# Optimization experiments

Measured on AMD Instinct MI355X. Metric: run time of the kernel, lower is better.

Reference implementation:

```python
import jax, jax.numpy as jnp
import numpy as np

B, S, D = 8, 2048, 1024
G, V = 2, 320          # num_groups, codebook_size
DG = D // G            # 512, per-group codevector dim
DIVERSITY_WEIGHT = 0.1


def setup_inputs() -> dict:
    key = jax.random.key(0)
    k1, k2, k3, k4 = jax.random.split(key, 4)
    hidden_states = jax.random.normal(k1, (B, S, D), dtype=jnp.float32)
    W = jax.random.normal(k2, (G * V, D), dtype=jnp.float32)   # weight_proj weight (torch Linear layout)
    b = jax.random.normal(k3, (G * V,), dtype=jnp.float32)     # weight_proj bias
    codevectors = jax.random.normal(k4, (1, G * V, DG), dtype=jnp.float32)
    return {"hidden_states": hidden_states, "W": W, "b": b, "codevectors": codevectors}


def reference(hidden_states, W, b, codevectors):
    batch, seq, _ = hidden_states.shape
    n_tok = batch * seq
    # weight_proj: [B,S,D] -> [B,S,G*V]
    logits = jnp.einsum("bsd,vd->bsv", hidden_states, W) + b
    logits_flat = logits.reshape(n_tok * G, V)
    # eval path: hard argmax codevector selection
    codevector_idx = jnp.argmax(logits_flat, axis=-1)          # [n_tok*G]
    probs = jax.nn.one_hot(codevector_idx, V, dtype=logits.dtype)  # exact one-hot, [n_tok*G, V]
    probs_g = probs.reshape(n_tok, G, V)
    # perplexity over marginal code usage (mask_time_indices=None)
    marginal = probs_g.mean(axis=0)                            # [G, V]
    perplexity = jnp.exp(-jnp.sum(marginal * jnp.log(marginal + 1e-7), axis=-1)).sum()
    # codevector lookup: one-hot @ codebook == gather of row g*V + idx_g
    idx2 = codevector_idx.reshape(n_tok, G)                    # [n_tok, G]
    cb = codevectors.reshape(G * V, DG)
    rows = idx2 + jnp.arange(G, dtype=idx2.dtype) * V          # global codebook rows
    gathered = jnp.take(cb, rows, axis=0)                      # [n_tok, G, DG]
    out = gathered.reshape(batch, seq, G * DG)                 # [B, S, D]
    # faithful to original (buggy) reshape: view(batch, num_groups, seq)
    idx_out = codevector_idx.reshape(batch, G, seq)
    num_codevectors = G * V
    diversity_loss = (num_codevectors - perplexity) / num_codevectors * DIVERSITY_WEIGHT
    return out, idx_out, diversity_loss
```

## Files before the change

kernel.cpp:

```cpp
#include <hip/hip_runtime.h>
#include <hip/hip_bf16.h>
#include <math.h>
#include <stdint.h>

#define BATCH 8
#define SEQ   2048
#define DMODEL 1024
#define GROUPS 2
#define VOCAB 320
#define NOUT  (GROUPS*VOCAB)
#define DG    (DMODEL/GROUPS)
#define NTOK  (BATCH*SEQ)
#define NPAIR (NTOK*GROUPS)
#define NCHUNK 10

#define MARGIN 4.0f
#define NEG_INF (-3.0e38f)

typedef __attribute__((ext_vector_type(8))) short short8;
typedef __attribute__((ext_vector_type(8))) unsigned short ushort8;
typedef __attribute__((ext_vector_type(4))) float f32x4;

__device__ __forceinline__ unsigned short f2bf(float f) {
    __hip_bfloat16 h = __float2bfloat16(f);
    return *reinterpret_cast<unsigned short*>(&h);
}
__device__ __forceinline__ float bf2f(unsigned short u) {
    unsigned int x = ((unsigned int)u) << 16;
    return __uint_as_float(x);
}

__device__ __forceinline__ void async16(const void* gptr, const void* lptr) {
    __builtin_amdgcn_global_load_lds(
        (const __attribute__((address_space(1))) unsigned int*)(unsigned long long)(uintptr_t)gptr,
        (__attribute__((address_space(3))) unsigned int*)(unsigned int)(uintptr_t)lptr,
        16, 0, 0);
}

#define NX4 (NTOK*DMODEL/4)
#define NW4 (NOUT*DMODEL/4)
__global__ __launch_bounds__(256) void convert_kernel(
    const float* __restrict__ X, const float* __restrict__ W,
    unsigned short* __restrict__ Xb, unsigned short* __restrict__ Wb,
    int* __restrict__ nAmb)
{
    int i = blockIdx.x * 256 + threadIdx.x;
    if (i == 0) *nAmb = 0;
    const float4* src;
    ushort4* dst;
    int j;
    if (i < NX4) { src = (const float4*)X; dst = (ushort4*)Xb; j = i; }
    else         { src = (const float4*)W; dst = (ushort4*)Wb; j = i - NX4; if (j >= NW4) return; }
    float4 v = src[j];
    ushort4 u;
    u.x = f2bf(v.x); u.y = f2bf(v.y); u.z = f2bf(v.z); u.w = f2bf(v.w);
    dst[j] = u;
}

__global__ __launch_bounds__(256) void gemm_bf16_kernel(
    const unsigned short* __restrict__ Xb,
    const unsigned short* __restrict__ Wb,
    const float* __restrict__ bias,
    unsigned short* __restrict__ logits,
    float* __restrict__ rec_m1,
    float* __restrict__ rec_m2,
    int*   __restrict__ rec_id)
{
    __shared__ __align__(16) unsigned short As[128 * 32];
    __shared__ __align__(16) unsigned short Bs[64 * 32];

    const int tid  = threadIdx.x;
    const int lane = tid & 63;
    const int wave = tid >> 6;
    const int m0 = blockIdx.x * 128;
    const int n0 = blockIdx.y * 64;
    const int wm = wave * 32;

    f32x4 acc[2][4];
    #pragma unroll
    for (int a = 0; a < 2; a++)
        #pragma unroll
        for (int b = 0; b < 4; b++)
            acc[a][b] = (f32x4)0.0f;

    int aoff[2], loffA[2], boff, loffB;
    #pragma unroll
    for (int j = 0; j < 2; j++) {
        int p = tid + j * 256;
        int r = p >> 2, s = p & 3;
        int c = s ^ ((r >> 1) & 3);
        aoff[j] = (m0 + r) * DMODEL + c * 8;
        loffA[j] = p * 8;
    }
    {
        int p = tid;
        int r = p >> 2, s = p & 3;
        int c = s ^ ((r >> 1) & 3);
        boff = (n0 + r) * DMODEL + c * 8;
        loffB = p * 8;
    }

    int afrag[2], bfrag[4];
    {
        int rho = lane & 15, h = lane >> 4;
        #pragma unroll
        for (int mi = 0; mi < 2; mi++) {
            int r = wm + mi * 16 + rho;
            afrag[mi] = (4 * r + (h ^ ((r >> 1) & 3))) * 8;
        }
        #pragma unroll
        for (int ni = 0; ni < 4; ni++) {
            int rn = ni * 16 + rho;
            bfrag[ni] = (4 * rn + (h ^ ((rn >> 1) & 3))) * 8;
        }
    }

    for (int k0 = 0; k0 < DMODEL; k0 += 32) {
        async16(Xb + aoff[0] + k0, As + loffA[0]);
        async16(Xb + aoff[1] + k0, As + loffA[1]);
        async16(Wb + boff + k0, Bs + loffB);
        __syncthreads();

        short8 af[2], bf[4];
        #pragma unroll
        for (int mi = 0; mi < 2; mi++) af[mi] = *(const short8*)&As[afrag[mi]];
        #pragma unroll
        for (int ni = 0; ni < 4; ni++) bf[ni] = *(const short8*)&Bs[bfrag[ni]];
        #pragma unroll
        for (int mi = 0; mi < 2; mi++)
            #pragma unroll
            for (int ni = 0; ni < 4; ni++)
                acc[mi][ni] = __builtin_amdgcn_mfma_f32_16x16x32_bf16(
                    af[mi], bf[ni], acc[mi][ni], 0, 0, 0);
        __syncthreads();
    }

    const int colb = n0 + (lane & 15);
    const int rowb = m0 + wm + (lane >> 4) * 4;
    const int chunk = blockIdx.y;
    float bv[4];
    #pragma unroll
    for (int ni = 0; ni < 4; ni++) bv[ni] = bias[colb + ni * 16];

    #pragma unroll
    for (int mi = 0; mi < 2; mi++) {
        #pragma unroll
        for (int p = 0; p < 4; p++) {
            const int row = rowb + mi * 16 + p;
            float m1 = acc[mi][0][p] + bv[0];
            float m2 = NEG_INF;
            int i1 = colb;
            logits[row * NOUT + colb] = f2bf(m1);
            #pragma unroll
            for (int ni = 1; ni < 4; ni++) {
                float v = acc[mi][ni][p] + bv[ni];
                logits[row * NOUT + colb + ni * 16] = f2bf(v);
                if (v > m1) { m2 = m1; m1 = v; i1 = colb + ni * 16; }
                else        { m2 = fmaxf(m2, v); }
            }
            #pragma unroll
            for (int off = 1; off < 16; off <<= 1) {
                float om1 = __shfl_xor(m1, off);
                float om2 = __shfl_xor(m2, off);
                int   oi  = __shfl_xor(i1, off);
                float nm2 = fmaxf(fmaxf(m2, om2), fminf(m1, om1));
                if (om1 > m1 || (om1 == m1 && oi < i1)) { m1 = om1; i1 = oi; }
                m2 = nm2;
            }
            if ((lane & 15) == 0) {
                rec_m1[row * NCHUNK + chunk] = m1;
                rec_m2[row * NCHUNK + chunk] = m2;
                rec_id[row * NCHUNK + chunk] = i1;
            }
        }
    }
}

__global__ __launch_bounds__(256) void reduce_kernel(
    const float* __restrict__ rec_m1, const float* __restrict__ rec_m2,
    const int* __restrict__ rec_id,
    float* __restrict__ out_idx,
    unsigned long long* __restrict__ list, int* __restrict__ nAmb)
{
    const int pair = blockIdx.x * 256 + threadIdx.x;
    const int token = pair >> 1;
    const int g = pair & 1;
    const int base = token * NCHUNK + g * 5;

    float m1[5], m2s, M;
    int cstar = 0;
    #pragma unroll
    for (int c = 0; c < 5; c++) m1[c] = rec_m1[base + c];
    M = m1[0];
    #pragma unroll
    for (int c = 1; c < 5; c++)
        if (m1[c] > M) { M = m1[c]; cstar = c; }
    m2s = rec_m2[base + cstar];

    const float thr = M - MARGIN;
    bool amb = (m2s >= thr);
    #pragma unroll
    for (int c = 0; c < 5; c++)
        if (c != cstar && m1[c] >= thr) amb = true;

    if (!amb) {
        out_idx[pair] = (float)(rec_id[base + cstar] - g * VOCAB);
    } else {
        out_idx[pair] = -1.0f;
    }

    unsigned long long mask = __ballot(amb);
    if (mask) {
        const int lane = threadIdx.x & 63;
        const int leader = __ffsll((long long)mask) - 1;
        int basepos = 0;
        if (lane == leader) basepos = atomicAdd(nAmb, (int)__popcll(mask));
        basepos = __shfl(basepos, leader);
        if (amb) {
            int off = __popcll(mask & ((1ull << lane) - 1ull));
            list[basepos + off] =
                ((unsigned long long)__float_as_uint(M) << 32) | (unsigned int)pair;
        }
    }
}

__global__ __launch_bounds__(256) void resolve_kernel(
    const float* __restrict__ X, const float* __restrict__ W,
    const float* __restrict__ bias,
    const unsigned short* __restrict__ logits,
    const unsigned long long* __restrict__ list, const int* __restrict__ nAmb,
    float* __restrict__ out_idx)
{
    const int lane  = threadIdx.x & 63;
    const int wglob = (blockIdx.x * 256 + threadIdx.x) >> 6;
    const int nwav  = gridDim.x * 4;
    const int n     = *nAmb;

    for (int slot = wglob; slot < n; slot += nwav) {
        const unsigned long long e = list[slot];
        const int pair  = (int)(e & 0xFFFFFFFFull);
        const float M   = __uint_as_float((unsigned int)(e >> 32));
        const int token = pair >> 1;
        const int g     = pair & 1;

        const float4* xr = (const float4*)(X + (size_t)token * DMODEL);
        float4 xv[4];
        #pragma unroll
        for (int q = 0; q < 4; q++) xv[q] = xr[lane + 64 * q];

        const unsigned short* lp = logits + token * NOUT + g * VOCAB;
        const bool have = (lane < 40);
        ushort8 u = (ushort8)0;
        if (have) u = *(const ushort8*)(lp + lane * 8);

        const float thr = M - MARGIN;
        float best = NEG_INF;
        int bestcol = 0;

        #pragma unroll
        for (int j = 0; j < 8; j++) {
            bool c = have && (bf2f(u[j]) >= thr);
            unsigned long long mask = __ballot(c);
            while (mask) {
                const int b = __ffsll((long long)mask) - 1;
                mask &= mask - 1;
                const int col = b * 8 + j;
                const float4* wr = (const float4*)(W + (size_t)(g * VOCAB + col) * DMODEL);
                float acc = 0.0f;
                #pragma unroll
                for (int q = 0; q < 4; q++) {
                    float4 bb = wr[lane + 64 * q];
                    acc = fmaf(xv[q].x, bb.x, acc);
                    acc = fmaf(xv[q].y, bb.y, acc);
                    acc = fmaf(xv[q].z, bb.z, acc);
                    acc = fmaf(xv[q].w, bb.w, acc);
                }
                #pragma unroll
                for (int off = 32; off >= 1; off >>= 1)
                    acc += __shfl_xor(acc, off);
                const float logit = acc + bias[g * VOCAB + col];
                if (logit > best || (logit == best && col < bestcol)) {
                    best = logit; bestcol = col;
                }
            }
        }
        if (lane == 0) out_idx[pair] = (float)bestcol;
    }
}

__global__ __launch_bounds__(256) void gather_kernel(
    const float* __restrict__ cb,
    const float* __restrict__ out_idx,
    float* __restrict__ out)
{
    __shared__ int gidx[32];
    const int t0 = blockIdx.x * 16;
    const int tid = threadIdx.x;

    if (tid < 32) {
        const int pair = t0 * 2 + tid;
        const int g = pair & 1;
        const int col = (int)out_idx[pair];
        gidx[tid] = g * VOCAB + col;
    }
    __syncthreads();

    #pragma unroll 4
    for (int i = 0; i < 16; i++) {
        const int token = t0 + i;
        const int gg = tid >> 7;
        const float4* src = (const float4*)(cb + (size_t)gidx[i * 2 + gg] * DG);
        ((float4*)(out + (size_t)token * DMODEL))[tid] = src[tid & 127];
    }
}

__global__ __launch_bounds__(256) void diversity_kernel(
    const float* __restrict__ out_idx, float* __restrict__ out_scalar)
{
    __shared__ int lhist[NOUT];
    __shared__ float s0[256], s1[256];
    const int tid = threadIdx.x;
    for (int i = tid; i < NOUT; i += 256) lhist[i] = 0;
    __syncthreads();

    const float4* oi4 = (const float4*)out_idx;
    for (int i = tid; i < NPAIR / 4; i += 256) {
        float4 v = oi4[i];
        atomicAdd(&lhist[0 * VOCAB + (int)v.x], 1);
        atomicAdd(&lhist[1 * VOCAB + (int)v.y], 1);
        atomicAdd(&lhist[0 * VOCAB + (int)v.z], 1);
        atomicAdd(&lhist[1 * VOCAB + (int)v.w], 1);
    }
    __syncthreads();

    float a0 = 0.0f, a1 = 0.0f;
    for (int i = tid; i < NOUT; i += 256) {
        float m = (float)lhist[i] * (1.0f / (float)NTOK);
        float t = m * logf(m + 1e-7f);
        if (i < VOCAB) a0 += t; else a1 += t;
    }
    s0[tid] = a0; s1[tid] = a1;
    __syncthreads();
    for (int s = 128; s > 0; s >>= 1) {
        if (tid < s) { s0[tid] += s0[tid + s]; s1[tid] += s1[tid + s]; }
        __syncthreads();
    }
    if (tid == 0) {
        float perplexity = expf(-s0[0]) + expf(-s1[0]);
        *out_scalar = ((float)NOUT - perplexity) / (float)NOUT * 0.1f;
    }
}

extern "C" void kernel_launch(void* const* d_in, const int* in_sizes, int n_in,
                              void* d_out, int out_size, void* d_ws, size_t ws_size,
                              hipStream_t stream) {
    const float* X    = (const float*)d_in[0];
    const float* W    = (const float*)d_in[1];
    const float* bias = (const float*)d_in[2];
    const float* cb   = (const float*)d_in[3];

    float* out      = (float*)d_out;
    float* out_idx  = out + (size_t)NTOK * DMODEL;
    float* out_loss = out_idx + NPAIR;

    char* p = (char*)d_ws;
    unsigned short* Xb = (unsigned short*)p;      p += (size_t)NTOK * DMODEL * 2;
    unsigned short* Wb = (unsigned short*)p;      p += (size_t)NOUT * DMODEL * 2;
    unsigned short* logits = (unsigned short*)p;  p += (size_t)NTOK * NOUT * 2;
    float* rec_m1 = (float*)p;                    p += (size_t)NTOK * NCHUNK * 4;
    float* rec_m2 = (float*)p;                    p += (size_t)NTOK * NCHUNK * 4;
    int*   rec_id = (int*)p;                      p += (size_t)NTOK * NCHUNK * 4;
    unsigned long long* list = (unsigned long long*)p; p += (size_t)NPAIR * 8;
    int* nAmb = (int*)p;                          p += 256;

    convert_kernel<<<(NX4 + NW4) / 256, 256, 0, stream>>>(X, W, Xb, Wb, nAmb);

    dim3 ggrid(NTOK / 128, NOUT / 64);
    gemm_bf16_kernel<<<ggrid, 256, 0, stream>>>(Xb, Wb, bias, logits,
                                                rec_m1, rec_m2, rec_id);

    reduce_kernel<<<NPAIR / 256, 256, 0, stream>>>(rec_m1, rec_m2, rec_id,
                                                   out_idx, list, nAmb);

    resolve_kernel<<<2048, 256, 0, stream>>>(X, W, bias, logits, list, nAmb,
                                             out_idx);

    gather_kernel<<<NTOK / 16, 256, 0, stream>>>(cb, out_idx, out);

    diversity_kernel<<<1, 256, 0, stream>>>(out_idx, out_loss);
}
```

Baseline: 209.7 us.

## Enlarge GEMM tile to 128x128 and fuse reduce, resolve and gather kernels

The GEMM block tile grows from 128x64 to 128x128, with each wave computing a 64x64 sub-tile. This raises MFMA work per LDS load and halves the number of blocks along N. The separate reduce, ambiguous-resolve and gather kernels are merged into one finalize kernel that handles 64 pairs per block: it decides each argmax, resolves ambiguous cases locally through shared memory, then gathers codevectors. This drops the global ambiguity list, the atomic counter and two launches, but the ambiguous work is now spread unevenly across blocks, and the larger tile uses more accumulator registers.

```diff
diff --git a/kernel.cpp b/kernel.cpp
--- a/kernel.cpp
+++ b/kernel.cpp
@@ -41,11 +41,9 @@
 #define NW4 (NOUT*DMODEL/4)
 __global__ __launch_bounds__(256) void convert_kernel(
     const float* __restrict__ X, const float* __restrict__ W,
-    unsigned short* __restrict__ Xb, unsigned short* __restrict__ Wb,
-    int* __restrict__ nAmb)
+    unsigned short* __restrict__ Xb, unsigned short* __restrict__ Wb)
 {
     int i = blockIdx.x * 256 + threadIdx.x;
-    if (i == 0) *nAmb = 0;
     const float4* src;
     ushort4* dst;
     int j;
@@ -67,67 +65,62 @@
     int*   __restrict__ rec_id)
 {
     __shared__ __align__(16) unsigned short As[128 * 32];
-    __shared__ __align__(16) unsigned short Bs[64 * 32];
+    __shared__ __align__(16) unsigned short Bs[128 * 32];
 
     const int tid  = threadIdx.x;
     const int lane = tid & 63;
     const int wave = tid >> 6;
     const int m0 = blockIdx.x * 128;
-    const int n0 = blockIdx.y * 64;
-    const int wm = wave * 32;
-
-    f32x4 acc[2][4];
+    const int n0 = blockIdx.y * 128;
+    const int wm = (wave & 1) * 64;
+    const int wn = (wave >> 1) * 64;
+
+    f32x4 acc[4][4];
     #pragma unroll
-    for (int a = 0; a < 2; a++)
+    for (int a = 0; a < 4; a++)
         #pragma unroll
         for (int b = 0; b < 4; b++)
             acc[a][b] = (f32x4)0.0f;
 
-    int aoff[2], loffA[2], boff, loffB;
+    int aoff[2], boff[2], loff[2];
     #pragma unroll
     for (int j = 0; j < 2; j++) {
         int p = tid + j * 256;
         int r = p >> 2, s = p & 3;
         int c = s ^ ((r >> 1) & 3);
         aoff[j] = (m0 + r) * DMODEL + c * 8;
-        loffA[j] = p * 8;
-    }
-    {
-        int p = tid;
-        int r = p >> 2, s = p & 3;
-        int c = s ^ ((r >> 1) & 3);
-        boff = (n0 + r) * DMODEL + c * 8;
-        loffB = p * 8;
-    }
-
-    int afrag[2], bfrag[4];
+        boff[j] = (n0 + r) * DMODEL + c * 8;
+        loff[j] = p * 8;
+    }
+
+    int afrag[4], bfrag[4];
     {
         int rho = lane & 15, h = lane >> 4;
         #pragma unroll
-        for (int mi = 0; mi < 2; mi++) {
+        for (int mi = 0; mi < 4; mi++) {
             int r = wm + mi * 16 + rho;
             afrag[mi] = (4 * r + (h ^ ((r >> 1) & 3))) * 8;
-        }
-        #pragma unroll
-        for (int ni = 0; ni < 4; ni++) {
-            int rn = ni * 16 + rho;
-            bfrag[ni] = (4 * rn + (h ^ ((rn >> 1) & 3))) * 8;
+            int rn = wn + mi * 16 + rho;
+            bfrag[mi] = (4 * rn + (h ^ ((rn >> 1) & 3))) * 8;
         }
     }
 
     for (int k0 = 0; k0 < DMODEL; k0 += 32) {
-        async16(Xb + aoff[0] + k0, As + loffA[0]);
-        async16(Xb + aoff[1] + k0, As + loffA[1]);
-        async16(Wb + boff + k0, Bs + loffB);
+        #pragma unroll
+        for (int j = 0; j < 2; j++) {
+            async16(Xb + aoff[j] + k0, As + loff[j]);
+            async16(Wb + boff[j] + k0, Bs + loff[j]);
+        }
         __syncthreads();
 
-        short8 af[2], bf[4];
-        #pragma unroll
-        for (int mi = 0; mi < 2; mi++) af[mi] = *(const short8*)&As[afrag[mi]];
-        #pragma unroll
-        for (int ni = 0; ni < 4; ni++) bf[ni] = *(const short8*)&Bs[bfrag[ni]];
-        #pragma unroll
-        for (int mi = 0; mi < 2; mi++)
+        short8 af[4], bf[4];
+        #pragma unroll
+        for (int i = 0; i < 4; i++) {
+            af[i] = *(const short8*)&As[afrag[i]];
+            bf[i] = *(const short8*)&Bs[bfrag[i]];
+        }
+        #pragma unroll
+        for (int mi = 0; mi < 4; mi++)
             #pragma unroll
             for (int ni = 0; ni < 4; ni++)
                 acc[mi][ni] = __builtin_amdgcn_mfma_f32_16x16x32_bf16(
@@ -135,15 +128,15 @@
         __syncthreads();
     }
 
-    const int colb = n0 + (lane & 15);
+    const int colb = n0 + wn + (lane & 15);
     const int rowb = m0 + wm + (lane >> 4) * 4;
-    const int chunk = blockIdx.y;
+    const int chunk = (n0 + wn) >> 6;
     float bv[4];
     #pragma unroll
     for (int ni = 0; ni < 4; ni++) bv[ni] = bias[colb + ni * 16];
 
     #pragma unroll
-    for (int mi = 0; mi < 2; mi++) {
+    for (int mi = 0; mi < 4; mi++) {
         #pragma unroll
         for (int p = 0; p < 4; p++) {
             const int row = rowb + mi * 16 + p;
@@ -176,82 +169,80 @@
     }
 }
 
-__global__ __launch_bounds__(256) void reduce_kernel(
-    const float* __restrict__ rec_m1, const float* __restrict__ rec_m2,
-    const int* __restrict__ rec_id,
-    float* __restrict__ out_idx,
-    unsigned long long* __restrict__ list, int* __restrict__ nAmb)
-{
-    const int pair = blockIdx.x * 256 + threadIdx.x;
-    const int token = pair >> 1;
-    const int g = pair & 1;
-    const int base = token * NCHUNK + g * 5;
-
-    float m1[5], m2s, M;
-    int cstar = 0;
-    #pragma unroll
-    for (int c = 0; c < 5; c++) m1[c] = rec_m1[base + c];
-    M = m1[0];
-    #pragma unroll
-    for (int c = 1; c < 5; c++)
-        if (m1[c] > M) { M = m1[c]; cstar = c; }
-    m2s = rec_m2[base + cstar];
-
-    const float thr = M - MARGIN;
-    bool amb = (m2s >= thr);
-    #pragma unroll
-    for (int c = 0; c < 5; c++)
-        if (c != cstar && m1[c] >= thr) amb = true;
-
-    if (!amb) {
-        out_idx[pair] = (float)(rec_id[base + cstar] - g * VOCAB);
-    } else {
-        out_idx[pair] = -1.0f;
-    }
-
-    unsigned long long mask = __ballot(amb);
-    if (mask) {
-        const int lane = threadIdx.x & 63;
-        const int leader = __ffsll((long long)mask) - 1;
-        int basepos = 0;
-        if (lane == leader) basepos = atomicAdd(nAmb, (int)__popcll(mask));
-        basepos = __shfl(basepos, leader);
-        if (amb) {
-            int off = __popcll(mask & ((1ull << lane) - 1ull));
-            list[basepos + off] =
-                ((unsigned long long)__float_as_uint(M) << 32) | (unsigned int)pair;
-        }
-    }
-}
-
-__global__ __launch_bounds__(256) void resolve_kernel(
+__global__ __launch_bounds__(256) void finalize_kernel(
     const float* __restrict__ X, const float* __restrict__ W,
     const float* __restrict__ bias,
     const unsigned short* __restrict__ logits,
-    const unsigned long long* __restrict__ list, const int* __restrict__ nAmb,
-    float* __restrict__ out_idx)
+    const float* __restrict__ rec_m1, const float* __restrict__ rec_m2,
+    const int* __restrict__ rec_id,
+    const float* __restrict__ cb,
+    float* __restrict__ out, float* __restrict__ out_idx)
 {
-    const int lane  = threadIdx.x & 63;
-    const int wglob = (blockIdx.x * 256 + threadIdx.x) >> 6;
-    const int nwav  = gridDim.x * 4;
-    const int n     = *nAmb;
-
-    for (int slot = wglob; slot < n; slot += nwav) {
-        const unsigned long long e = list[slot];
-        const int pair  = (int)(e & 0xFFFFFFFFull);
-        const float M   = __uint_as_float((unsigned int)(e >> 32));
+    __shared__ int   lcol[64];
+    __shared__ float lM[64];
+    __shared__ int   lamb[64];
+    __shared__ int   slcnt;
+
+    const int tid   = threadIdx.x;
+    const int lane  = tid & 63;
+    const int wave  = tid >> 6;
+    const int pair0 = blockIdx.x * 64;
+
+    if (tid < 64) {
+        const int pair  = pair0 + tid;
         const int token = pair >> 1;
         const int g     = pair & 1;
+        const int base  = token * NCHUNK + g * 5;
+
+        float m1[5], M;
+        int cstar = 0;
+        #pragma unroll
+        for (int c = 0; c < 5; c++) m1[c] = rec_m1[base + c];
+        M = m1[0];
+        #pragma unroll
+        for (int c = 1; c < 5; c++)
+            if (m1[c] > M) { M = m1[c]; cstar = c; }
+        const float m2s = rec_m2[base + cstar];
+
+        const float thr = M - MARGIN;
+        bool amb = (m2s >= thr);
+        #pragma unroll
+        for (int c = 0; c < 5; c++)
+            if (c != cstar && m1[c] >= thr) amb = true;
+
+        if (!amb) {
+            const int gcol = rec_id[base + cstar];
+            lcol[tid] = gcol;
+            out_idx[pair] = (float)(gcol - g * VOCAB);
+        } else {
+            lM[tid] = M;
+        }
+        unsigned long long mask = __ballot(amb);
+        if (amb) {
+            int off = __popcll(mask & ((1ull << tid) - 1ull));
+            lamb[off] = tid;
+        }
+        if (tid == 0) slcnt = (int)__popcll(mask);
+    }
+    __syncthreads();
+    const int nloc = slcnt;
+
+    for (int s = wave; s < nloc; s += 4) {
+        const int lp    = lamb[s];
+        const int pair  = pair0 + lp;
+        const float M   = lM[lp];
+        const int token = pair >> 1;
+        const int g     = pair & 1;
 
         const float4* xr = (const float4*)(X + (size_t)token * DMODEL);
         float4 xv[4];
         #pragma unroll
         for (int q = 0; q < 4; q++) xv[q] = xr[lane + 64 * q];
 
-        const unsigned short* lp = logits + token * NOUT + g * VOCAB;
+        const unsigned short* lp_ = logits + token * NOUT + g * VOCAB;
         const bool have = (lane < 40);
         ushort8 u = (ushort8)0;
-        if (have) u = *(const ushort8*)(lp + lane * 8);
+        if (have) u = *(const ushort8*)(lp_ + lane * 8);
 
         const float thr = M - MARGIN;
         float best = NEG_INF;
@@ -284,32 +275,18 @@
                 }
             }
         }
-        if (lane == 0) out_idx[pair] = (float)bestcol;
-    }
-}
-
-__global__ __launch_bounds__(256) void gather_kernel(
-    const float* __restrict__ cb,
-    const float* __restrict__ out_idx,
-    float* __restrict__ out)
-{
-    __shared__ int gidx[32];
-    const int t0 = blockIdx.x * 16;
-    const int tid = threadIdx.x;
-
-    if (tid < 32) {
-        const int pair = t0 * 2 + tid;
-        const int g = pair & 1;
-        const int col = (int)out_idx[pair];
-        gidx[tid] = g * VOCAB + col;
+        if (lane == 0) {
+            lcol[lp] = g * VOCAB + bestcol;
+            out_idx[pair] = (float)bestcol;
+        }
     }
     __syncthreads();
 
     #pragma unroll 4
-    for (int i = 0; i < 16; i++) {
-        const int token = t0 + i;
+    for (int i = 0; i < 32; i++) {
+        const int token = pair0 / 2 + i;
         const int gg = tid >> 7;
-        const float4* src = (const float4*)(cb + (size_t)gidx[i * 2 + gg] * DG);
+        const float4* src = (const float4*)(cb + (size_t)lcol[i * 2 + gg] * DG);
         ((float4*)(out + (size_t)token * DMODEL))[tid] = src[tid & 127];
     }
 }
@@ -370,22 +347,16 @@
     float* rec_m1 = (float*)p;                    p += (size_t)NTOK * NCHUNK * 4;
     float* rec_m2 = (float*)p;                    p += (size_t)NTOK * NCHUNK * 4;
     int*   rec_id = (int*)p;                      p += (size_t)NTOK * NCHUNK * 4;
-    unsigned long long* list = (unsigned long long*)p; p += (size_t)NPAIR * 8;
-    int* nAmb = (int*)p;                          p += 256;
-
-    convert_kernel<<<(NX4 + NW4) / 256, 256, 0, stream>>>(X, W, Xb, Wb, nAmb);
-
-    dim3 ggrid(NTOK / 128, NOUT / 64);
+
+    convert_kernel<<<(NX4 + NW4) / 256, 256, 0, stream>>>(X, W, Xb, Wb);
+
+    dim3 ggrid(NTOK / 128, NOUT / 128);
     gemm_bf16_kernel<<<ggrid, 256, 0, stream>>>(Xb, Wb, bias, logits,
                                                 rec_m1, rec_m2, rec_id);
 
-    reduce_kernel<<<NPAIR / 256, 256, 0, stream>>>(rec_m1, rec_m2, rec_id,
-                                                   out_idx, list, nAmb);
-
-    resolve_kernel<<<2048, 256, 0, stream>>>(X, W, bias, logits, list, nAmb,
-                                             out_idx);
-
-    gather_kernel<<<NTOK / 16, 256, 0, stream>>>(cb, out_idx, out);
+    finalize_kernel<<<NPAIR / 64, 256, 0, stream>>>(X, W, bias, logits,
+                                                    rec_m1, rec_m2, rec_id,
+                                                    cb, out, out_idx);
 
     diversity_kernel<<<1, 256, 0, stream>>>(out_idx, out_loss);
 }
```

New measurement: 196.3 us. 6.4% less time.
